# Performance work log

Measured on AMD Instinct MI355X. Metric: run time of the kernel, lower is better.

The kernel has to match this reference:

```python
import jax, jax.numpy as jnp
import numpy as np

N = 100000
C = 32            # channels per degree (shape_in == shape_out == 32)
NI = C * C        # flattened Gram-matrix size = n_input = n_hidden
LN_EPS = 1e-5
SLOPE = 0.01      # LeakyReLU default negative slope


def _ln(x, g, b):
    mu = jnp.mean(x, axis=-1, keepdims=True)
    var = jnp.var(x, axis=-1, keepdims=True)  # biased, matches torch LayerNorm
    return (x - mu) * jax.lax.rsqrt(var + LN_EPS) * g + b


def _lrelu(x):
    return jnp.where(x >= 0, x, SLOPE * x)


def _gal(v, g1, b1, w1, g2, b2, w2, bias2):
    # v: [N, ch_in, m]
    n, ci, _ = v.shape
    dot = jnp.einsum('nac,nbc->nab', v, v).reshape(n, ci * ci)  # Gram matrix
    dot = jnp.sign(dot) * jnp.maximum(jnp.abs(dot), 1e-12)
    h = _lrelu(_ln(dot, g1, b1)) @ w1.T           # [N, ch_in*ch_out]
    h = _lrelu(_ln(h, g2, b2)) @ w2.T + bias2      # [N, ch_in*ch_out]
    attn = jax.nn.softmax(h.reshape(n, -1, ci), axis=-1)  # [N, ch_out, ch_in]
    return jnp.einsum('nab,nbc->nac', attn, v)     # [N, ch_out, m]


def _mk_type_params(key):
    ks = jax.random.split(key, 3)
    bound = np.sqrt(6.0 / NI)  # kaiming_uniform_, fan_in=NI
    return dict(
        ln1_g=jnp.ones((NI,), jnp.float32),
        ln1_b=jnp.zeros((NI,), jnp.float32),
        w1=jax.random.uniform(ks[0], (NI, NI), jnp.float32, -bound, bound),
        ln2_g=jnp.ones((NI,), jnp.float32),
        ln2_b=jnp.zeros((NI,), jnp.float32),
        w2=jax.random.uniform(ks[1], (NI, NI), jnp.float32, -bound, bound),
        b2=jax.random.uniform(ks[2], (NI,), jnp.float32, -1.0 / C, 1.0 / C),
    )


def setup_inputs():
    key = jax.random.key(0)
    k0, k1, kp0, kp1 = jax.random.split(key, 4)
    d = {
        'f0': jax.random.normal(k0, (N, C, 1), jnp.float32),
        'f1': jax.random.normal(k1, (N, C, 3), jnp.float32),
    }
    for tag, kk in (('0', kp0), ('1', kp1)):
        p = _mk_type_params(kk)
        for name, val in p.items():
            d[f'{name}_{tag}'] = val
    return d


def reference(f0, f1,
              ln1_g_0, ln1_b_0, w1_0, ln2_g_0, ln2_b_0, w2_0, b2_0,
              ln1_g_1, ln1_b_1, w1_1, ln2_g_1, ln2_b_1, w2_1, b2_1):
    out0 = _gal(f0, ln1_g_0, ln1_b_0, w1_0, ln2_g_0, ln2_b_0, w2_0, b2_0)
    out1 = _gal(f1, ln1_g_1, ln1_b_1, w1_1, ln2_g_1, ln2_b_1, w2_1, b2_1)
    return (out0, out1)
```

## Files before the change

### kernel.cpp

```cpp
#include <hip/hip_runtime.h>

#define NN     100000
#define NB     1563
#define LN_EPS 1e-5f
#define SLOPE  0.01f

typedef __bf16 bf16x8 __attribute__((ext_vector_type(8)));
typedef float  f32x4  __attribute__((ext_vector_type(4)));
typedef unsigned short u16;
typedef unsigned int   u32;

union Pack8 { uint4 u4; bf16x8 bf; u16 s[8]; };

__device__ __forceinline__ u16 f2bf(float x){
    u32 b = __float_as_uint(x);
    b += 0x7fffu + ((b >> 16) & 1u);
    return (u16)(b >> 16);
}

__global__ __launch_bounds__(1024) void prep_weights(
    const float* __restrict__ wa, const float* __restrict__ wb,
    const float* __restrict__ wc, const float* __restrict__ wd,
    u16* __restrict__ dst)
{
    int m = blockIdx.y;
    const float* src = (m==0)? wa : (m==1)? wb : (m==2)? wc : wd;
    u16* d = dst + (size_t)m * (1024u*1024u);
    int tid = blockIdx.x * blockDim.x + threadIdx.x;
    int sub = tid & 3;
    int row = (tid >> 2) & 1023;
    int kb  = tid >> 12;
    const float4* s4 = (const float4*)(src + row*1024 + kb*32 + sub*8);
    float4 a = s4[0], b = s4[1];
    Pack8 p;
    p.s[0]=f2bf(a.x); p.s[1]=f2bf(a.y); p.s[2]=f2bf(a.z); p.s[3]=f2bf(a.w);
    p.s[4]=f2bf(b.x); p.s[5]=f2bf(b.y); p.s[6]=f2bf(b.z); p.s[7]=f2bf(b.w);
    ((uint4*)d)[(kb*1024 + row)*4 + sub] = p.u4;
}

__device__ __forceinline__ void gemm_quad1(
    const u16* __restrict__ Wp, const u16* xs,
    int C0, int lane15, int q, f32x4 acc[4][4])
{
    const uint4* bb = (const uint4*)Wp + (C0 + lane15)*4 + q;
    const uint4* ab = (const uint4*)xs + q*64 + lane15;
    #pragma unroll
    for (int t=0; t<4; ++t)
      #pragma unroll
      for (int rt=0; rt<4; ++rt)
        acc[t][rt] = (f32x4){0.f,0.f,0.f,0.f};
    #pragma unroll 2
    for (int ks=0; ks<32; ++ks){
        Pack8 b[4], a[4];
        #pragma unroll
        for (int t=0; t<4; ++t) b[t].u4 = bb[ks*4096 + t*64];
        #pragma unroll
        for (int rt=0; rt<4; ++rt) a[rt].u4 = ab[ks*256 + rt*16];
        #pragma unroll
        for (int t=0; t<4; ++t)
          #pragma unroll
          for (int rt=0; rt<4; ++rt)
            acc[t][rt] = __builtin_amdgcn_mfma_f32_16x16x32_bf16(a[rt].bf, b[t].bf, acc[t][rt], 0,0,0);
    }
}

template<int MDIM>
__device__ __forceinline__ void gal_body(
    const int blk, char* smem,
    const float* __restrict__ f,
    const float* __restrict__ ln1g, const float* __restrict__ ln1b,
    const float* __restrict__ ln2g, const float* __restrict__ ln2b,
    const float* __restrict__ b2,
    const u16* __restrict__ Wp1, const u16* __restrict__ Wp2,
    float* __restrict__ outp)
{
    constexpr int VSTR = 32*MDIM + 4;
    constexpr int SBS  = 64*32 + 4;
    u16*   xs    = (u16*)smem;
    float* sbuf  = (float*)smem;
    float* vbuf  = (float*)smem + 32832;
    float* stats = (float*)smem + 32832 + 64*VSTR;

    const int tid    = threadIdx.x;
    const int lane   = tid & 63;
    const int wv     = tid >> 6;
    const int lane15 = lane & 15;
    const int q      = lane >> 4;
    const int node0  = blk * 64;

    if (tid < 128) stats[tid] = 0.f;
    {
        float4* vbuf4 = (float4*)vbuf;
        const int gv4  = node0*8*MDIM;
        const int lim4 = NN*8*MDIM;
        for (int i = tid; i < 64*8*MDIM; i += 1024){
            int nd = i / (8*MDIM);
            int r4 = i - nd*(8*MDIM);
            float4 val = (gv4 + i < lim4) ? ((const float4*)f)[gv4 + i]
                                          : (float4){0.f,0.f,0.f,0.f};
            vbuf4[nd*(VSTR/4) + r4] = val;
        }
    }
    __syncthreads();

    {
        const int n = tid >> 4;
        const int j = tid & 15;
        const float* vn = vbuf + n*VSTR;
        float va[2][MDIM];
        #pragma unroll
        for (int c=0;c<MDIM;++c){ va[0][c]=vn[(j*2)*MDIM+c]; va[1][c]=vn[(j*2+1)*MDIM+c]; }
        float sum=0.f, ssum=0.f;
        #pragma unroll
        for (int b=0;b<32;++b){
            float d0=0.f, d1=0.f;
            #pragma unroll
            for (int c=0;c<MDIM;++c){ float vb = vn[b*MDIM+c]; d0 += va[0][c]*vb; d1 += va[1][c]*vb; }
            sum += d0+d1; ssum += d0*d0 + d1*d1;
        }
        #pragma unroll
        for (int st=1; st<16; st<<=1){ sum += __shfl_xor(sum, st); ssum += __shfl_xor(ssum, st); }
        float mu   = sum * (1.f/1024.f);
        float rstd = rsqrtf(ssum*(1.f/1024.f) - mu*mu + LN_EPS);
        #pragma unroll
        for (int jb=0;jb<8;++jb){
            Pack8 p;
            const int ai = jb >> 2;
            #pragma unroll
            for (int l=0;l<8;++l){
                int b = (jb*8+l) & 31;
                float d = 0.f;
                #pragma unroll
                for (int c=0;c<MDIM;++c) d += va[ai][c]*vn[b*MDIM+c];
                int k = j*64 + jb*8 + l;
                float x = (d - mu)*rstd*ln1g[k] + ln1b[k];
                x = (x >= 0.f)? x : SLOPE*x;
                p.s[l] = f2bf(x);
            }
            ((uint4*)xs)[(j*8+jb)*64 + n] = p.u4;
        }
    }
    __syncthreads();

    {
        f32x4 acc[4][4];
        gemm_quad1(Wp1, xs, wv*64, lane15, q, acc);
        {
            float p_[16], pp_[16];
            #pragma unroll
            for (int idx=0; idx<16; ++idx){
                int rt = idx>>2, rr = idx&3;
                float s=0.f, s2=0.f;
                #pragma unroll
                for (int t=0; t<4; ++t){ float h = acc[t][rt][rr]; s += h; s2 += h*h; }
                p_[idx] = s; pp_[idx] = s2;
            }
            #pragma unroll
            for (int m=8; m>=1; m>>=1){
                const bool hi = (lane15 & m) != 0;
                #pragma unroll
                for (int i=0; i<m; ++i){
                    float sp = hi ? p_[i]  : p_[i+m];
                    float kp = hi ? p_[i+m]  : p_[i];
                    p_[i]  = kp + __shfl_xor(sp, m);
                    float sq = hi ? pp_[i] : pp_[i+m];
                    float kq = hi ? pp_[i+m] : pp_[i];
                    pp_[i] = kq + __shfl_xor(sq, m);
                }
            }
            int nd = (lane15>>2)*16 + q*4 + (lane15&3);
            atomicAdd(&stats[2*nd],   p_[0]);
            atomicAdd(&stats[2*nd+1], pp_[0]);
        }
        __syncthreads();

        float g2c[4], b2c[4];
        #pragma unroll
        for (int t=0; t<4; ++t){
            int col = wv*64 + t*16 + lane15;
            g2c[t] = ln2g[col];
            b2c[t] = ln2b[col];
        }
        #pragma unroll
        for (int rt=0; rt<4; ++rt)
          #pragma unroll
          for (int rr=0; rr<4; ++rr){
            int nd = rt*16 + q*4 + rr;
            float mu   = stats[2*nd]*(1.f/1024.f);
            float rstd = rsqrtf(stats[2*nd+1]*(1.f/1024.f) - mu*mu + LN_EPS);
            #pragma unroll
            for (int t=0; t<4; ++t){
                float h = acc[t][rt][rr];
                float x = (h - mu)*rstd*g2c[t] + b2c[t];
                x = (x >= 0.f)? x : SLOPE*x;
                int col = wv*64 + t*16 + lane15;
                xs[(col>>3)*512 + nd*8 + (col&7)] = f2bf(x);
            }
          }
    }
    __syncthreads();

    {
        f32x4 acc[4][4];
        gemm_quad1(Wp2, xs, wv*64, lane15, q, acc);
        float bias[4];
        #pragma unroll
        for (int t=0; t<4; ++t)
            bias[t] = b2[wv*64 + t*16 + lane15];
        __syncthreads();

        const int nd_c = tid >> 4;
        const int s_c  = tid & 15;
        float keep[2][MDIM];

        #pragma unroll
        for (int ps=0; ps<2; ++ps){
            #pragma unroll
            for (int ctl=0; ctl<2; ++ctl){
                const int t = ps*2 + ctl;
                #pragma unroll
                for (int rt=0; rt<4; ++rt)
                  #pragma unroll
                  for (int rr=0; rr<4; ++rr){
                    int nd = rt*16 + q*4 + rr;
                    sbuf[wv*SBS + nd*32 + ctl*16 + lane15] = acc[t][rt][rr] + bias[t];
                  }
            }
            __syncthreads();
            {
                const float* hp = sbuf + s_c*SBS + nd_c*32;
                float e[32];
                #pragma unroll
                for (int r=0;r<8;++r){
                    float4 v4 = ((const float4*)hp)[r];
                    e[4*r]=v4.x; e[4*r+1]=v4.y; e[4*r+2]=v4.z; e[4*r+3]=v4.w;
                }
                float mx = e[0];
                #pragma unroll
                for (int b=1;b<32;++b) mx = fmaxf(mx, e[b]);
                float sm = 0.f;
                #pragma unroll
                for (int b=0;b<32;++b){ e[b] = __expf(e[b]-mx); sm += e[b]; }
                float inv = 1.f / sm;
                float oacc[MDIM];
                #pragma unroll
                for (int c=0;c<MDIM;++c) oacc[c]=0.f;
                const float4* vr = (const float4*)(vbuf + nd_c*VSTR);
                #pragma unroll
                for (int r=0; r<8*MDIM; ++r){
                    float4 v4 = vr[r];
                    #pragma unroll
                    for (int t=0;t<4;++t){
                        const int fi = 4*r+t;
                        const int b  = fi/MDIM;
                        const int c  = fi - b*MDIM;
                        float comp = (t==0)?v4.x:(t==1)?v4.y:(t==2)?v4.z:v4.w;
                        oacc[c] += e[b]*comp;
                    }
                }
                #pragma unroll
                for (int c=0;c<MDIM;++c) keep[ps][c] = oacc[c]*inv;
            }
            __syncthreads();
        }

        {
            float* img = sbuf;
            #pragma unroll
            for (int c=0;c<MDIM;++c){
                img[nd_c*(32*MDIM) + (2*s_c  )*MDIM + c] = keep[0][c];
                img[nd_c*(32*MDIM) + (2*s_c+1)*MDIM + c] = keep[1][c];
            }
        }
        __syncthreads();

        {
            const float4* img4 = (const float4*)sbuf;
            float4* out4 = (float4*)(outp + (size_t)node0*(32*MDIM));
            constexpr int NPV = 8*MDIM;
            for (int i = tid; i < 64*NPV; i += 1024){
                int nd = (MDIM==1) ? (i >> 3) : (i / NPV);
                if (node0 + nd < NN) out4[i] = img4[i];
            }
        }
    }
}

__global__ __launch_bounds__(1024, 4) void gal_fused_all(
    const float* __restrict__ f0, const float* __restrict__ f1,
    const float* __restrict__ ln1g0, const float* __restrict__ ln1b0,
    const float* __restrict__ ln2g0, const float* __restrict__ ln2b0,
    const float* __restrict__ b2_0,
    const float* __restrict__ ln1g1, const float* __restrict__ ln1b1,
    const float* __restrict__ ln2g1, const float* __restrict__ ln2b1,
    const float* __restrict__ b2_1,
    const u16* __restrict__ wp, float* __restrict__ out)
{
    extern __shared__ char smem[];
    const int gid = blockIdx.x;
    if (gid < NB)
        gal_body<3>(gid, smem, f1, ln1g1, ln1b1, ln2g1, ln2b1, b2_1,
                    wp + 2097152,  wp + 3145728, out + (size_t)NN*32);
    else
        gal_body<1>(gid - NB, smem, f0, ln1g0, ln1b0, ln2g0, ln2b0, b2_0,
                    wp,            wp + 1048576, out);
}

extern "C" void kernel_launch(void* const* d_in, const int* in_sizes, int n_in,
                              void* d_out, int out_size, void* d_ws, size_t ws_size,
                              hipStream_t stream)
{
    const float* f0    = (const float*)d_in[0];
    const float* f1    = (const float*)d_in[1];
    const float* ln1g0 = (const float*)d_in[2];
    const float* ln1b0 = (const float*)d_in[3];
    const float* w1_0  = (const float*)d_in[4];
    const float* ln2g0 = (const float*)d_in[5];
    const float* ln2b0 = (const float*)d_in[6];
    const float* w2_0  = (const float*)d_in[7];
    const float* b2_0  = (const float*)d_in[8];
    const float* ln1g1 = (const float*)d_in[9];
    const float* ln1b1 = (const float*)d_in[10];
    const float* w1_1  = (const float*)d_in[11];
    const float* ln2g1 = (const float*)d_in[12];
    const float* ln2b1 = (const float*)d_in[13];
    const float* w2_1  = (const float*)d_in[14];
    const float* b2_1  = (const float*)d_in[15];
    float* out = (float*)d_out;
    u16* wp = (u16*)d_ws;

    const int smem = (32832 + 64*(32*3+4) + 128)*4;
    (void)hipFuncSetAttribute(reinterpret_cast<const void*>(&gal_fused_all),
                              hipFuncAttributeMaxDynamicSharedMemorySize, smem);

    prep_weights<<<dim3(128,4), 1024, 0, stream>>>(w1_0, w2_0, w1_1, w2_1, wp);
    gal_fused_all<<<2*NB, 1024, smem, stream>>>(f0, f1,
        ln1g0, ln1b0, ln2g0, ln2b0, b2_0,
        ln1g1, ln1b1, ln2g1, ln2b1, b2_1,
        wp, out);
}
```

Measured before the change: 1.331 ms.

## Switch both GEMMs to 32x32x16 MFMA with matching weight layout and epilogue

Replaces the 16x16x32 bf16 MFMA tiling with 32x32x16 MFMA instructions, so each wave issues 4 larger MFMAs per k-step instead of 16 small ones and needs fewer operand loads per FLOP. The packed weight layout produced by prep_weights is reordered to suit the new operand fetch pattern. The LayerNorm statistics reduction, the LN2 writeback and the softmax staging are all remapped to the 32x32 accumulator layout. The softmax staging now has half the waves write each pass, which changes the output column ordering. The cost is larger per-lane accumulators, which adds register pressure, plus a more complex row-index mapping.

Result: slower. 1.672 ms (+25.6%).

```diff
diff --git a/kernel.cpp b/kernel.cpp
--- a/kernel.cpp
+++ b/kernel.cpp
@@ -6,7 +6,7 @@
 #define SLOPE  0.01f
 
 typedef __bf16 bf16x8 __attribute__((ext_vector_type(8)));
-typedef float  f32x4  __attribute__((ext_vector_type(4)));
+typedef float  f32x16 __attribute__((ext_vector_type(16)));
 typedef unsigned short u16;
 typedef unsigned int   u32;
 
@@ -35,32 +35,32 @@
     Pack8 p;
     p.s[0]=f2bf(a.x); p.s[1]=f2bf(a.y); p.s[2]=f2bf(a.z); p.s[3]=f2bf(a.w);
     p.s[4]=f2bf(b.x); p.s[5]=f2bf(b.y); p.s[6]=f2bf(b.z); p.s[7]=f2bf(b.w);
-    ((uint4*)d)[(kb*1024 + row)*4 + sub] = p.u4;
-}
-
-__device__ __forceinline__ void gemm_quad1(
+    ((uint4*)d)[(kb*4 + sub)*1024 + row] = p.u4;
+}
+
+__device__ __forceinline__ void gemm_quad32(
     const u16* __restrict__ Wp, const u16* xs,
-    int C0, int lane15, int q, f32x4 acc[4][4])
-{
-    const uint4* bb = (const uint4*)Wp + (C0 + lane15)*4 + q;
-    const uint4* ab = (const uint4*)xs + q*64 + lane15;
+    int C0, int lane31, int hi, f32x16 acc[2][2])
+{
+    const uint4* bb = (const uint4*)Wp + hi*1024 + C0 + lane31;
+    const uint4* ab = (const uint4*)xs + hi*64  + lane31;
     #pragma unroll
-    for (int t=0; t<4; ++t)
+    for (int t=0; t<2; ++t)
       #pragma unroll
-      for (int rt=0; rt<4; ++rt)
-        acc[t][rt] = (f32x4){0.f,0.f,0.f,0.f};
+      for (int rt=0; rt<2; ++rt)
+        #pragma unroll
+        for (int e=0; e<16; ++e) acc[t][rt][e] = 0.f;
     #pragma unroll 2
-    for (int ks=0; ks<32; ++ks){
-        Pack8 b[4], a[4];
-        #pragma unroll
-        for (int t=0; t<4; ++t) b[t].u4 = bb[ks*4096 + t*64];
-        #pragma unroll
-        for (int rt=0; rt<4; ++rt) a[rt].u4 = ab[ks*256 + rt*16];
-        #pragma unroll
-        for (int t=0; t<4; ++t)
-          #pragma unroll
-          for (int rt=0; rt<4; ++rt)
-            acc[t][rt] = __builtin_amdgcn_mfma_f32_16x16x32_bf16(a[rt].bf, b[t].bf, acc[t][rt], 0,0,0);
+    for (int ks=0; ks<64; ++ks){
+        Pack8 b0, b1, a0, a1;
+        b0.u4 = bb[ks*2048];
+        b1.u4 = bb[ks*2048 + 32];
+        a0.u4 = ab[ks*128];
+        a1.u4 = ab[ks*128 + 32];
+        acc[0][0] = __builtin_amdgcn_mfma_f32_32x32x16_bf16(a0.bf, b0.bf, acc[0][0], 0,0,0);
+        acc[0][1] = __builtin_amdgcn_mfma_f32_32x32x16_bf16(a1.bf, b0.bf, acc[0][1], 0,0,0);
+        acc[1][0] = __builtin_amdgcn_mfma_f32_32x32x16_bf16(a0.bf, b1.bf, acc[1][0], 0,0,0);
+        acc[1][1] = __builtin_amdgcn_mfma_f32_32x32x16_bf16(a1.bf, b1.bf, acc[1][1], 0,0,0);
     }
 }
 
@@ -84,8 +84,8 @@
     const int tid    = threadIdx.x;
     const int lane   = tid & 63;
     const int wv     = tid >> 6;
-    const int lane15 = lane & 15;
-    const int q      = lane >> 4;
+    const int lane31 = lane & 31;
+    const int hi     = lane >> 5;
     const int node0  = blk * 64;
 
     if (tid < 128) stats[tid] = 0.f;
@@ -143,57 +143,70 @@
     __syncthreads();
 
     {
-        f32x4 acc[4][4];
-        gemm_quad1(Wp1, xs, wv*64, lane15, q, acc);
+        f32x16 acc[2][2];
+        gemm_quad32(Wp1, xs, wv*64, lane31, hi, acc);
+        const int nd_f = (lane31>>4)*32 + (lane31&3) + 8*((lane31>>2)&3) + 4*hi;
         {
-            float p_[16], pp_[16];
-            #pragma unroll
-            for (int idx=0; idx<16; ++idx){
-                int rt = idx>>2, rr = idx&3;
-                float s=0.f, s2=0.f;
-                #pragma unroll
-                for (int t=0; t<4; ++t){ float h = acc[t][rt][rr]; s += h; s2 += h*h; }
-                p_[idx] = s; pp_[idx] = s2;
-            }
-            #pragma unroll
-            for (int m=8; m>=1; m>>=1){
-                const bool hi = (lane15 & m) != 0;
+            float p_[32];
+            #pragma unroll
+            for (int idx=0; idx<32; ++idx){
+                int rt = idx>>4, rg = idx&15;
+                p_[idx] = acc[0][rt][rg] + acc[1][rt][rg];
+            }
+            #pragma unroll
+            for (int m=16; m>=1; m>>=1){
+                const bool up = (lane31 & m) != 0;
                 #pragma unroll
                 for (int i=0; i<m; ++i){
-                    float sp = hi ? p_[i]  : p_[i+m];
-                    float kp = hi ? p_[i+m]  : p_[i];
-                    p_[i]  = kp + __shfl_xor(sp, m);
-                    float sq = hi ? pp_[i] : pp_[i+m];
-                    float kq = hi ? pp_[i+m] : pp_[i];
-                    pp_[i] = kq + __shfl_xor(sq, m);
-                }
-            }
-            int nd = (lane15>>2)*16 + q*4 + (lane15&3);
-            atomicAdd(&stats[2*nd],   p_[0]);
-            atomicAdd(&stats[2*nd+1], pp_[0]);
+                    float sp = up ? p_[i]   : p_[i+m];
+                    float kp = up ? p_[i+m] : p_[i];
+                    p_[i] = kp + __shfl_xor(sp, m);
+                }
+            }
+            atomicAdd(&stats[2*nd_f], p_[0]);
+        }
+        {
+            float p_[32];
+            #pragma unroll
+            for (int idx=0; idx<32; ++idx){
+                int rt = idx>>4, rg = idx&15;
+                float h0 = acc[0][rt][rg], h1 = acc[1][rt][rg];
+                p_[idx] = h0*h0 + h1*h1;
+            }
+            #pragma unroll
+            for (int m=16; m>=1; m>>=1){
+                const bool up = (lane31 & m) != 0;
+                #pragma unroll
+                for (int i=0; i<m; ++i){
+                    float sp = up ? p_[i]   : p_[i+m];
+                    float kp = up ? p_[i+m] : p_[i];
+                    p_[i] = kp + __shfl_xor(sp, m);
+                }
+            }
+            atomicAdd(&stats[2*nd_f+1], p_[0]);
         }
         __syncthreads();
 
-        float g2c[4], b2c[4];
-        #pragma unroll
-        for (int t=0; t<4; ++t){
-            int col = wv*64 + t*16 + lane15;
+        float g2c[2], b2c[2];
+        #pragma unroll
+        for (int t=0; t<2; ++t){
+            int col = wv*64 + t*32 + lane31;
             g2c[t] = ln2g[col];
             b2c[t] = ln2b[col];
         }
         #pragma unroll
-        for (int rt=0; rt<4; ++rt)
+        for (int rt=0; rt<2; ++rt)
           #pragma unroll
-          for (int rr=0; rr<4; ++rr){
-            int nd = rt*16 + q*4 + rr;
+          for (int rg=0; rg<16; ++rg){
+            int nd = rt*32 + (rg&3) + 8*((rg>>2)&3) + 4*hi;
             float mu   = stats[2*nd]*(1.f/1024.f);
             float rstd = rsqrtf(stats[2*nd+1]*(1.f/1024.f) - mu*mu + LN_EPS);
             #pragma unroll
-            for (int t=0; t<4; ++t){
-                float h = acc[t][rt][rr];
+            for (int t=0; t<2; ++t){
+                float h = acc[t][rt][rg];
                 float x = (h - mu)*rstd*g2c[t] + b2c[t];
                 x = (x >= 0.f)? x : SLOPE*x;
-                int col = wv*64 + t*16 + lane15;
+                int col = wv*64 + t*32 + lane31;
                 xs[(col>>3)*512 + nd*8 + (col&7)] = f2bf(x);
             }
           }
@@ -201,39 +214,42 @@
     __syncthreads();
 
     {
-        f32x4 acc[4][4];
-        gemm_quad1(Wp2, xs, wv*64, lane15, q, acc);
-        float bias[4];
-        #pragma unroll
-        for (int t=0; t<4; ++t)
-            bias[t] = b2[wv*64 + t*16 + lane15];
+        f32x16 acc[2][2];
+        gemm_quad32(Wp2, xs, wv*64, lane31, hi, acc);
+        float bias[2];
+        #pragma unroll
+        for (int t=0; t<2; ++t)
+            bias[t] = b2[wv*64 + t*32 + lane31];
         __syncthreads();
 
         const int nd_c = tid >> 4;
         const int s_c  = tid & 15;
+        const int myr  = wv >> 3;
         float keep[2][MDIM];
 
         #pragma unroll
-        for (int ps=0; ps<2; ++ps){
-            #pragma unroll
-            for (int ctl=0; ctl<2; ++ctl){
-                const int t = ps*2 + ctl;
-                #pragma unroll
-                for (int rt=0; rt<4; ++rt)
-                  #pragma unroll
-                  for (int rr=0; rr<4; ++rr){
-                    int nd = rt*16 + q*4 + rr;
-                    sbuf[wv*SBS + nd*32 + ctl*16 + lane15] = acc[t][rt][rr] + bias[t];
-                  }
+        for (int r=0; r<2; ++r){
+            if (myr == r){
+                #pragma unroll
+                for (int t=0; t<2; ++t){
+                    const int slot = (wv&7)*2 + t;
+                    #pragma unroll
+                    for (int rt=0; rt<2; ++rt)
+                      #pragma unroll
+                      for (int rg=0; rg<16; ++rg){
+                        int nd = rt*32 + (rg&3) + 8*((rg>>2)&3) + 4*hi;
+                        sbuf[slot*SBS + nd*32 + lane31] = acc[t][rt][rg] + bias[t];
+                      }
+                }
             }
             __syncthreads();
             {
                 const float* hp = sbuf + s_c*SBS + nd_c*32;
                 float e[32];
                 #pragma unroll
-                for (int r=0;r<8;++r){
-                    float4 v4 = ((const float4*)hp)[r];
-                    e[4*r]=v4.x; e[4*r+1]=v4.y; e[4*r+2]=v4.z; e[4*r+3]=v4.w;
+                for (int rr=0;rr<8;++rr){
+                    float4 v4 = ((const float4*)hp)[rr];
+                    e[4*rr]=v4.x; e[4*rr+1]=v4.y; e[4*rr+2]=v4.z; e[4*rr+3]=v4.w;
                 }
                 float mx = e[0];
                 #pragma unroll
@@ -247,11 +263,11 @@
                 for (int c=0;c<MDIM;++c) oacc[c]=0.f;
                 const float4* vr = (const float4*)(vbuf + nd_c*VSTR);
                 #pragma unroll
-                for (int r=0; r<8*MDIM; ++r){
-                    float4 v4 = vr[r];
+                for (int rr=0; rr<8*MDIM; ++rr){
+                    float4 v4 = vr[rr];
                     #pragma unroll
                     for (int t=0;t<4;++t){
-                        const int fi = 4*r+t;
+                        const int fi = 4*rr+t;
                         const int b  = fi/MDIM;
                         const int c  = fi - b*MDIM;
                         float comp = (t==0)?v4.x:(t==1)?v4.y:(t==2)?v4.z:v4.w;
@@ -259,7 +275,7 @@
                     }
                 }
                 #pragma unroll
-                for (int c=0;c<MDIM;++c) keep[ps][c] = oacc[c]*inv;
+                for (int c=0;c<MDIM;++c) keep[r][c] = oacc[c]*inv;
             }
             __syncthreads();
         }
@@ -268,8 +284,8 @@
             float* img = sbuf;
             #pragma unroll
             for (int c=0;c<MDIM;++c){
-                img[nd_c*(32*MDIM) + (2*s_c  )*MDIM + c] = keep[0][c];
-                img[nd_c*(32*MDIM) + (2*s_c+1)*MDIM + c] = keep[1][c];
+                img[nd_c*(32*MDIM) + (     s_c)*MDIM + c] = keep[0][c];
+                img[nd_c*(32*MDIM) + (16 + s_c)*MDIM + c] = keep[1][c];
             }
         }
         __syncthreads();
```
